# Performance work log

Hardware: AMD Instinct MI355X
Metric: run time of the kernel (lower is better)

The kernel has to match this reference:

```python
import math
import jax, jax.numpy as jnp
import numpy as np

# ---- matryoshka config (matches init_kwargs) ----
NUM_HEADS = 16
KV_GROUPS = 4
KV_REPEATS = NUM_HEADS // KV_GROUPS
QK_SIZES = [32, 64, 128]      # output_sizes // num_heads
HEAD_SIZES = [32, 64, 128]
D_MODEL = 2048
NEG_INF = -1e9


def _heads_reorder_indices(num_heads, sizes, reverse=False):
    parts = [[] for _ in range(num_heads)]
    offset, prev = 0, 0
    for size in sizes:
        seg = size - prev
        for h in range(num_heads):
            parts[h].append(np.arange(offset, offset + seg))
            offset += seg
        prev = size
    reorder = np.concatenate([a for head in parts for a in head])
    if reverse:
        rev = np.empty_like(reorder)
        rev[reorder] = np.arange(len(reorder))
        reorder = rev
    return jnp.asarray(reorder, dtype=jnp.int32)

Q_REORDER = _heads_reorder_indices(NUM_HEADS, QK_SIZES)
K_REORDER = _heads_reorder_indices(KV_GROUPS, QK_SIZES)
V_REORDER = _heads_reorder_indices(KV_GROUPS, HEAD_SIZES)
O_REORDER = _heads_reorder_indices(NUM_HEADS, HEAD_SIZES, reverse=True)


def setup_inputs() -> dict:
    key = jax.random.key(0)
    ks = jax.random.split(key, 9)
    B, S = 2, 1024
    dq = NUM_HEADS * QK_SIZES[-1]      # 2048
    dkv_q = KV_GROUPS * QK_SIZES[-1]   # 512
    dkv_v = KV_GROUPS * HEAD_SIZES[-1] # 512
    dout = NUM_HEADS * HEAD_SIZES[-1]  # 2048
    s = 0.02
    return {
        "x": jax.random.normal(ks[0], (B, S, D_MODEL), jnp.float32),
        "mask": jnp.tril(jnp.ones((S, S), jnp.bool_)),
        "Wq": jax.random.normal(ks[1], (D_MODEL, dq), jnp.float32) * s,
        "bq": jnp.zeros((dq,), jnp.float32),
        "Wk": jax.random.normal(ks[2], (D_MODEL, dkv_q), jnp.float32) * s,
        "bk": jnp.zeros((dkv_q,), jnp.float32),
        "Wv": jax.random.normal(ks[3], (D_MODEL, dkv_v), jnp.float32) * s,
        "bv": jnp.zeros((dkv_v,), jnp.float32),
        "Wo": jax.random.normal(ks[4], (dout, D_MODEL), jnp.float32) * s,
        "bo": jnp.zeros((D_MODEL,), jnp.float32),
    }


def reference(x, mask, Wq, bq, Wk, bk, Wv, bv, Wo, bo):
    B, S, _ = x.shape
    H, G, R = NUM_HEADS, KV_GROUPS, KV_REPEATS
    Dq, Dh = QK_SIZES[-1], HEAD_SIZES[-1]

    # matryoshka projections (full-size forward) + buffer-indexed reorder
    q = (x @ Wq + bq)[..., Q_REORDER]
    k = (x @ Wk + bk)[..., K_REORDER]
    v = (x @ Wv + bv)[..., V_REORDER]

    q = q.reshape(B, S, H, Dq).transpose(0, 2, 1, 3)   # [B,H,S,Dq]
    k = k.reshape(B, S, G, Dq).transpose(0, 2, 1, 3)   # [B,G,S,Dq]
    v = v.reshape(B, S, G, Dh).transpose(0, 2, 1, 3)   # [B,G,S,Dh]

    # GQA expansion: each group repeated kv_repeats times consecutively
    k = jnp.repeat(k, R, axis=1)  # [B,H,S,Dq]
    v = jnp.repeat(v, R, axis=1)  # [B,H,S,Dh]

    add_mask = jnp.where(mask, 0.0, NEG_INF).astype(x.dtype)  # [S,S]

    xs = []
    dp_cum = 0.0
    prev_qk, prev_hd = 0, 0
    for qk, hd in zip(QK_SIZES, HEAD_SIZES):
        # dot product over the NEW qk segment, accumulated over prefixes
        dp = jnp.einsum('bhqd,bhkd->bhqk', q[..., prev_qk:qk], k[..., prev_qk:qk])
        dp_cum = dp_cum + dp
        logits = dp_cum * (1.0 / math.sqrt(qk)) + add_mask
        attn = jax.nn.softmax(logits, axis=-1)
        # output only the NEW value segment for this nesting level
        xs.append(jnp.einsum('bhqk,bhkd->bhqd', attn, v[..., prev_hd:hd]))
        prev_qk, prev_hd = qk, hd

    out = jnp.concatenate(xs, axis=-1)                 # [B,H,S,Dh]
    out = out.transpose(0, 2, 1, 3).reshape(B, S, H * Dh)
    out = out[..., O_REORDER]
    return out @ Wo + bo
```

## Files before the change

kernel.cpp:

```cpp
#include <hip/hip_runtime.h>

typedef __attribute__((ext_vector_type(8))) __bf16 bf16x8;
typedef __attribute__((ext_vector_type(8))) unsigned short u16x8;
typedef __attribute__((ext_vector_type(4))) float f32x4;

#define XBOFF 0
#define WQKVOFF (XBOFF + 2048 * 2048)
#define WOOFF   (WQKVOFF + 3072 * 2048)
#define QOFF    (WOOFF + 2048 * 2048)
#define KOFF    (QOFF + 2048 * 2048)
#define VTOFF   (KOFF + 2048 * 512)
#define AOFF    (VTOFF + 2048 * 512)
__device__ __align__(16) ushort g_scratch[AOFF + 2048 * 2048];

__device__ __forceinline__ int nest_map(int n, int H) {
    int h = n >> 7, j = n & 127;
    if (j < 32) return h * 32 + j;
    if (j < 64) return H * 32 + h * 32 + (j - 32);
    return H * 64 + h * 64 + (j - 64);
}

__device__ __forceinline__ ushort f2bf(float f) {
    unsigned u = __builtin_bit_cast(unsigned, f);
    u += 0x7fffu + ((u >> 16) & 1u);
    return (ushort)(u >> 16);
}
__device__ __forceinline__ bf16x8 ld_frag(const ushort* p) {
    return __builtin_bit_cast(bf16x8, *(const u16x8*)p);
}
__device__ __forceinline__ void glds16(const ushort* g, ushort* s) {
    __builtin_amdgcn_global_load_lds(
        (const __attribute__((address_space(1))) void*)g,
        (__attribute__((address_space(3))) void*)s, 16, 0, 0);
}

__global__ __launch_bounds__(256) void prep_kernel(
    const float* __restrict__ x,
    const float* __restrict__ Wq, const float* __restrict__ Wk,
    const float* __restrict__ Wv, const float* __restrict__ Wo)
{
    const int bx = blockIdx.x;
    const int tid = threadIdx.x;

    if (bx < 2048) {
        size_t i = ((size_t)bx * 256 + tid) * 8;
        float4 f0 = *(const float4*)&x[i];
        float4 f1 = *(const float4*)&x[i + 4];
        union { uint4 v; ushort u[8]; } a;
        a.u[0] = f2bf(f0.x); a.u[1] = f2bf(f0.y); a.u[2] = f2bf(f0.z); a.u[3] = f2bf(f0.w);
        a.u[4] = f2bf(f1.x); a.u[5] = f2bf(f1.y); a.u[6] = f2bf(f1.z); a.u[7] = f2bf(f1.w);
        *(uint4*)&g_scratch[XBOFF + i] = a.v;
        return;
    }

    const float* W; int rowlen, H, mode, dstoff, t;
    if (bx < 3072)      { W = Wq; rowlen = 2048; H = 16; mode = 0; dstoff = WQKVOFF;               t = bx - 2048; }
    else if (bx < 3328) { W = Wk; rowlen = 512;  H = 4;  mode = 0; dstoff = WQKVOFF + 2048 * 2048; t = bx - 3072; }
    else if (bx < 3584) { W = Wv; rowlen = 512;  H = 4;  mode = 0; dstoff = WQKVOFF + 2560 * 2048; t = bx - 3328; }
    else                { W = Wo; rowlen = 2048; H = 16; mode = 1; dstoff = WOOFF;                 t = bx - 3584; }
    const int k0 = (t & 31) * 64;
    const int n0 = (t >> 5) * 64;

    __shared__ ushort T[64][66];
    const int r = tid >> 3, oct = tid & 7;

    #pragma unroll
    for (int rep = 0; rep < 2; ++rep) {
        int rr = r + rep * 32;
        int wrow = mode ? nest_map(k0 + rr, 16) : (k0 + rr);
        int wcol = mode ? (n0 + oct * 8) : nest_map(n0 + oct * 8, H);
        float4 f0 = *(const float4*)&W[(size_t)wrow * rowlen + wcol];
        float4 f1 = *(const float4*)&W[(size_t)wrow * rowlen + wcol + 4];
        ushort* d = &T[rr][oct * 8];
        d[0] = f2bf(f0.x); d[1] = f2bf(f0.y); d[2] = f2bf(f0.z); d[3] = f2bf(f0.w);
        d[4] = f2bf(f1.x); d[5] = f2bf(f1.y); d[6] = f2bf(f1.z); d[7] = f2bf(f1.w);
    }
    __syncthreads();
    #pragma unroll
    for (int rep = 0; rep < 2; ++rep) {
        int rr = r + rep * 32;
        union { uint4 v; ushort u[8]; } cv;
        #pragma unroll
        for (int i = 0; i < 8; ++i) cv.u[i] = T[oct * 8 + i][rr];
        *(uint4*)&g_scratch[dstoff + (size_t)(n0 + rr) * 2048 + k0 + oct * 8] = cv.v;
    }
}

__global__ __launch_bounds__(256) void gemm128_kernel(
    const float* __restrict__ b0, const float* __restrict__ b1,
    const float* __restrict__ b2, float* __restrict__ oext, int mode)
{
    __shared__ __align__(16) ushort SH[128 * 64 + 64 * 64];
    ushort* As = SH;
    ushort* Bs = SH + 128 * 64;

    const int gx = gridDim.x;
    const int nwg = gx * gridDim.y;
    const int id = blockIdx.x + gx * blockIdx.y;
    const int id2 = (id & 7) * (nwg >> 3) + (id >> 3);
    const int m_idx = id2 / gx;
    const int n_idx = id2 - m_idx * gx;
    const int n0 = n_idx * 64;
    const int m0 = m_idx * 128;

    const int tid = threadIdx.x;
    const int lane = tid & 63, wid = tid >> 6;
    const int wm = wid & 1, wn = wid >> 1;
    const int quad = lane >> 4, l16 = lane & 15;

    const ushort* A  = g_scratch + (mode ? AOFF : XBOFF);
    const ushort* Bt = g_scratch + (mode ? WOOFF : WQKVOFF);

    const bool vpath = (mode == 0) && (n0 >= 2560);
    const float* bias; ushort* outS = nullptr; int c0, oldim, H;
    if (mode == 1)      { bias = b0; c0 = n0; oldim = 2048; H = 0; }
    else if (n0 < 2048) { bias = b0; outS = g_scratch + QOFF; c0 = n0;        oldim = 2048; H = 16; }
    else if (n0 < 2560) { bias = b1; outS = g_scratch + KOFF; c0 = n0 - 2048; oldim = 512;  H = 4; }
    else                { bias = b2; outS = nullptr;          c0 = n0 - 2560; oldim = 512;  H = 4; }

    const int lrow = lane >> 3;
    const int lchunk = (lane & 7) ^ (lrow & 7);

    f32x4 acc[4][2];
    #pragma unroll
    for (int a = 0; a < 4; ++a)
        #pragma unroll
        for (int c = 0; c < 2; ++c) acc[a][c] = f32x4{0.f, 0.f, 0.f, 0.f};

    for (int kt = 0; kt < 32; ++kt) {
        const int k0 = kt * 64;
        #pragma unroll
        for (int it = 0; it < 4; ++it) {
            int rb = it * 32 + wid * 8;
            int r  = rb + lrow;
            glds16(&A[(size_t)(m0 + r) * 2048 + k0 + lchunk * 8], &As[rb * 64]);
        }
        #pragma unroll
        for (int it = 0; it < 2; ++it) {
            int rb = it * 32 + wid * 8;
            int r  = rb + lrow;
            glds16(&Bt[(size_t)(n0 + r) * 2048 + k0 + lchunk * 8], &Bs[rb * 64]);
        }
        __syncthreads();
        #pragma unroll
        for (int kc = 0; kc < 2; ++kc) {
            bf16x8 af[4], bf[2];
            #pragma unroll
            for (int s = 0; s < 4; ++s) {
                int ra = wm * 64 + s * 16 + l16;
                int ch = kc * 4 + quad;
                af[s] = ld_frag(&As[ra * 64 + ((ch ^ (ra & 7)) * 8)]);
            }
            #pragma unroll
            for (int s = 0; s < 2; ++s) {
                int rbv = wn * 32 + s * 16 + l16;
                int ch = kc * 4 + quad;
                bf[s] = ld_frag(&Bs[rbv * 64 + ((ch ^ (rbv & 7)) * 8)]);
            }
            #pragma unroll
            for (int sm = 0; sm < 4; ++sm)
                #pragma unroll
                for (int sn = 0; sn < 2; ++sn)
                    acc[sm][sn] = __builtin_amdgcn_mfma_f32_16x16x32_bf16(
                        af[sm], bf[sn], acc[sm][sn], 0, 0, 0);
        }
        __syncthreads();
    }

    if (vpath) {
        #pragma unroll
        for (int sm = 0; sm < 4; ++sm)
        #pragma unroll
        for (int sn = 0; sn < 2; ++sn)
        #pragma unroll
        for (int i = 0; i < 4; ++i) {
            int r = wm * 64 + sm * 16 + quad * 4 + i;
            int loc = wn * 32 + sn * 16 + l16;
            float v = acc[sm][sn][i] + bias[nest_map(c0 + loc, 4)];
            SH[loc * 128 + (r ^ ((loc & 7) << 3))] = f2bf(v);
        }
        __syncthreads();
        const int dloc = tid >> 2;
        const int qcol = (tid & 3) * 32;
        const int gg = c0 >> 7, din = (c0 & 127);
        const int bb = m0 >> 10, sb = m0 & 1023;
        ushort* vt = g_scratch + VTOFF;
        #pragma unroll
        for (int j = 0; j < 4; ++j) {
            int r = qcol + j * 8;
            uint4 v = *(uint4*)&SH[dloc * 128 + (r ^ ((dloc & 7) << 3))];
            *(uint4*)&vt[((size_t)((bb * 4 + gg) * 128 + din + dloc)) * 1024 + sb + r] = v;
        }
    } else {
        #pragma unroll
        for (int sm = 0; sm < 4; ++sm)
        #pragma unroll
        for (int sn = 0; sn < 2; ++sn)
        #pragma unroll
        for (int i = 0; i < 4; ++i) {
            int row = m0 + wm * 64 + sm * 16 + quad * 4 + i;
            int loc = wn * 32 + sn * 16 + l16;
            float v = acc[sm][sn][i];
            if (mode == 1) {
                oext[(size_t)row * 2048 + c0 + loc] = v + bias[c0 + loc];
            } else {
                v += bias[nest_map(c0 + loc, H)];
                outS[(size_t)row * oldim + c0 + loc] = f2bf(v);
            }
        }
    }
}

__global__ __launch_bounds__(256) void attn_kernel()
{
    const ushort* qb = g_scratch + QOFF;
    const ushort* kb = g_scratch + KOFF;
    const ushort* vt = g_scratch + VTOFF;
    ushort* att = g_scratch + AOFF;

    __shared__ __align__(16) ushort Ks[64 * 128];
    __shared__ __align__(16) ushort Vt[128 * 64];
    __shared__ __align__(16) ushort Ps[64 * 64];

    const int x = blockIdx.x, h = blockIdx.y, b = blockIdx.z;
    const int ks_half = x >> 1;
    const int qt = ((x ^ b) & 1) ? ks_half : 15 - ks_half;
    const int g = h >> 2;
    const int q0 = qt * 64;
    const int tid = threadIdx.x;
    const int lane = tid & 63, w = tid >> 6;
    const int quad = lane >> 4, l16 = lane & 15;

    bf16x8 qa[4];
    {
        const ushort* qrow =
            qb + ((size_t)((b * 1024 + q0 + w * 16 + l16) * 16 + h)) * 128;
        #pragma unroll
        for (int kc = 0; kc < 4; ++kc)
            qa[kc] = ld_frag(qrow + kc * 32 + quad * 8);
    }

    float m_s[3][4], l_s[3][4];
    #pragma unroll
    for (int l = 0; l < 3; ++l)
        #pragma unroll
        for (int i = 0; i < 4; ++i) { m_s[l][i] = -1e9f; l_s[l][i] = 0.0f; }
    f32x4 oacc[8];
    #pragma unroll
    for (int t2 = 0; t2 < 8; ++t2) oacc[t2] = f32x4{0.f, 0.f, 0.f, 0.f};
    const f32x4 fz = {0.f, 0.f, 0.f, 0.f};

    for (int kt = 0; kt <= qt; ++kt) {
        const int k0 = kt * 64;
        {
            int r16 = tid >> 4, oct16 = tid & 15;
            #pragma unroll
            for (int rep = 0; rep < 4; ++rep) {
                int row = r16 + rep * 16;
                *(uint4*)&Ks[row * 128 + ((oct16 ^ (row & 7)) * 8)] =
                    *(const uint4*)&kb[(size_t)((b * 1024 + k0 + row) * 4 + g) * 128 + oct16 * 8];
            }
            int oct = tid & 7, dr = tid >> 3;
            #pragma unroll
            for (int rep = 0; rep < 4; ++rep) {
                int d = dr + rep * 32;
                *(uint4*)&Vt[d * 64 + ((oct ^ (d & 7)) * 8)] =
                    *(const uint4*)&vt[((size_t)((b * 4 + g) * 128 + d)) * 1024 + k0 + oct * 8];
            }
        }
        __syncthreads();

        const bool diag = (kt == qt);

        f32x4 s0[4], s1[4], s2[4];
        __builtin_amdgcn_s_setprio(1);
        #pragma unroll
        for (int n = 0; n < 4; ++n) {
            int r = n * 16 + l16;
            s0[n] = __builtin_amdgcn_mfma_f32_16x16x32_bf16(
                qa[0], ld_frag(&Ks[r * 128 + (((0 + quad) ^ (r & 7)) * 8)]), fz, 0, 0, 0);
        }
        #pragma unroll
        for (int n = 0; n < 4; ++n) {
            int r = n * 16 + l16;
            s1[n] = __builtin_amdgcn_mfma_f32_16x16x32_bf16(
                qa[1], ld_frag(&Ks[r * 128 + (((4 + quad) ^ (r & 7)) * 8)]), s0[n], 0, 0, 0);
        }
        #pragma unroll
        for (int n = 0; n < 4; ++n) {
            int r = n * 16 + l16;
            s2[n] = __builtin_amdgcn_mfma_f32_16x16x32_bf16(
                qa[2], ld_frag(&Ks[r * 128 + (((8 + quad) ^ (r & 7)) * 8)]), s1[n], 0, 0, 0);
        }
        #pragma unroll
        for (int n = 0; n < 4; ++n) {
            int r = n * 16 + l16;
            s2[n] = __builtin_amdgcn_mfma_f32_16x16x32_bf16(
                qa[3], ld_frag(&Ks[r * 128 + (((12 + quad) ^ (r & 7)) * 8)]), s2[n], 0, 0, 0);
        }
        __builtin_amdgcn_s_setprio(0);

        float sv[3][4][4], mx[3][4];
        #pragma unroll
        for (int l = 0; l < 3; ++l)
            #pragma unroll
            for (int i = 0; i < 4; ++i) mx[l][i] = -1e9f;
        #pragma unroll
        for (int n = 0; n < 4; ++n)
            #pragma unroll
            for (int i = 0; i < 4; ++i) {
                bool msk = diag &&
                    (k0 + n * 16 + l16 > q0 + w * 16 + quad * 4 + i);
                float x0 = msk ? -1e9f : s0[n][i] * 0.1767766953f;
                float x1 = msk ? -1e9f : s1[n][i] * 0.125f;
                float x2 = msk ? -1e9f : s2[n][i] * 0.0883883476f;
                sv[0][n][i] = x0; mx[0][i] = fmaxf(mx[0][i], x0);
                sv[1][n][i] = x1; mx[1][i] = fmaxf(mx[1][i], x1);
                sv[2][n][i] = x2; mx[2][i] = fmaxf(mx[2][i], x2);
            }
        #pragma unroll
        for (int d = 1; d < 16; d <<= 1)
            #pragma unroll
            for (int l = 0; l < 3; ++l)
                #pragma unroll
                for (int i = 0; i < 4; ++i)
                    mx[l][i] = fmaxf(mx[l][i], __shfl_xor(mx[l][i], d, 64));
        float al[3][4], rs[3][4];
        #pragma unroll
        for (int l = 0; l < 3; ++l)
            #pragma unroll
            for (int i = 0; i < 4; ++i) {
                float mn = fmaxf(m_s[l][i], mx[l][i]);
                al[l][i] = __expf(m_s[l][i] - mn);
                m_s[l][i] = mn;
                rs[l][i] = 0.f;
            }
        #pragma unroll
        for (int n = 0; n < 4; ++n)
            #pragma unroll
            for (int l = 0; l < 3; ++l)
                #pragma unroll
                for (int i = 0; i < 4; ++i) {
                    float p = __expf(sv[l][n][i] - m_s[l][i]);
                    sv[l][n][i] = p;
                    rs[l][i] += p;
                }
        #pragma unroll
        for (int d = 1; d < 16; d <<= 1)
            #pragma unroll
            for (int l = 0; l < 3; ++l)
                #pragma unroll
                for (int i = 0; i < 4; ++i)
                    rs[l][i] += __shfl_xor(rs[l][i], d, 64);
        #pragma unroll
        for (int l = 0; l < 3; ++l)
            #pragma unroll
            for (int i = 0; i < 4; ++i)
                l_s[l][i] = l_s[l][i] * al[l][i] + rs[l][i];
        #pragma unroll
        for (int t = 0; t < 8; ++t) {
            int lvl = (t < 2) ? 0 : (t < 4) ? 1 : 2;
            #pragma unroll
            for (int i = 0; i < 4; ++i) oacc[t][i] *= al[lvl][i];
        }

        const int obase[3] = {0, 2, 4}, onts[3] = {2, 2, 4}, voffs[3] = {0, 32, 64};
        #pragma unroll
        for (int l = 0; l < 3; ++l) {
            #pragma unroll
            for (int n = 0; n < 4; ++n)
                #pragma unroll
                for (int i = 0; i < 4; ++i) {
                    int prow = w * 16 + quad * 4 + i;
                    int col = n * 16 + l16;
                    Ps[prow * 64 + ((((col >> 3) ^ (prow & 7)) << 3) | (col & 7))] =
                        f2bf(sv[l][n][i]);
                }
            __builtin_amdgcn_s_setprio(1);
            #pragma unroll
            for (int kc = 0; kc < 2; ++kc) {
                int prow = w * 16 + l16;
                bf16x8 pa = ld_frag(&Ps[prow * 64 + (((kc * 4 + quad) ^ (prow & 7)) * 8)]);
                #pragma unroll
                for (int t = 0; t < 4; ++t) {
                    if (t < onts[l]) {
                        int vd = voffs[l] + t * 16 + l16;
                        bf16x8 vf = ld_frag(&Vt[vd * 64 + (((kc * 4 + quad) ^ (vd & 7)) * 8)]);
                        oacc[obase[l] + t] = __builtin_amdgcn_mfma_f32_16x16x32_bf16(
                            pa, vf, oacc[obase[l] + t], 0, 0, 0);
                    }
                }
            }
            __builtin_amdgcn_s_setprio(0);
        }
        __syncthreads();
    }

    float inv[3][4];
    #pragma unroll
    for (int l = 0; l < 3; ++l)
        #pragma unroll
        for (int i = 0; i < 4; ++i) {
            float L = l_s[l][i];
            inv[l][i] = (L > 0.f) ? (1.0f / L) : 0.f;
        }
    #pragma unroll
    for (int t = 0; t < 8; ++t) {
        int lvl = (t < 2) ? 0 : (t < 4) ? 1 : 2;
        #pragma unroll
        for (int i = 0; i < 4; ++i) {
            int srow = q0 + w * 16 + quad * 4 + i;
            att[(size_t)((b * 1024 + srow) * 16 + h) * 128 + t * 16 + l16] =
                f2bf(oacc[t][i] * inv[lvl][i]);
        }
    }
}

extern "C" void kernel_launch(void* const* d_in, const int* in_sizes, int n_in,
                              void* d_out, int out_size, void* d_ws, size_t ws_size,
                              hipStream_t stream)
{
    const float* x  = (const float*)d_in[0];
    const float* Wq = (const float*)d_in[2];
    const float* bq = (const float*)d_in[3];
    const float* Wk = (const float*)d_in[4];
    const float* bk = (const float*)d_in[5];
    const float* Wv = (const float*)d_in[6];
    const float* bv = (const float*)d_in[7];
    const float* Wo = (const float*)d_in[8];
    const float* bo = (const float*)d_in[9];
    float* out = (float*)d_out;
    (void)d_ws; (void)ws_size;

    dim3 blk(256, 1, 1);
    hipLaunchKernelGGL(prep_kernel, dim3(4608), blk, 0, stream, x, Wq, Wk, Wv, Wo);
    hipLaunchKernelGGL(gemm128_kernel, dim3(48, 16), blk, 0, stream,
                       bq, bk, bv, (float*)nullptr, 0);
    hipLaunchKernelGGL(attn_kernel, dim3(16, 16, 2), blk, 0, stream);
    hipLaunchKernelGGL(gemm128_kernel, dim3(32, 16), blk, 0, stream,
                       bo, nullptr, nullptr, out, 1);
}
```

Before: 277.9 us.

## Split attention blocks into 32-row halves and compute row sums via MFMA

```diff
diff --git a/kernel.cpp b/kernel.cpp
--- a/kernel.cpp
+++ b/kernel.cpp
@@ -211,7 +211,7 @@
     }
 }
 
-__global__ __launch_bounds__(256) void attn_kernel()
+__global__ __launch_bounds__(128) void attn_kernel()
 {
     const ushort* qb = g_scratch + QOFF;
     const ushort* kb = g_scratch + KOFF;
@@ -220,13 +220,14 @@
 
     __shared__ __align__(16) ushort Ks[64 * 128];
     __shared__ __align__(16) ushort Vt[128 * 64];
-    __shared__ __align__(16) ushort Ps[64 * 64];
-
-    const int x = blockIdx.x, h = blockIdx.y, b = blockIdx.z;
-    const int ks_half = x >> 1;
-    const int qt = ((x ^ b) & 1) ? ks_half : 15 - ks_half;
+    __shared__ __align__(16) ushort Ps[32 * 64];
+
+    const int x = blockIdx.x, y = blockIdx.y, b = blockIdx.z;
+    const int h = x >> 1, half = x & 1;
+    const int qt = (y < 8) ? (15 - y) : (y - 8);
     const int g = h >> 2;
     const int q0 = qt * 64;
+    const int r0 = q0 + half * 32;
     const int tid = threadIdx.x;
     const int lane = tid & 63, w = tid >> 6;
     const int quad = lane >> 4, l16 = lane & 15;
@@ -234,7 +235,7 @@
     bf16x8 qa[4];
     {
         const ushort* qrow =
-            qb + ((size_t)((b * 1024 + q0 + w * 16 + l16) * 16 + h)) * 128;
+            qb + ((size_t)((b * 1024 + r0 + w * 16 + l16) * 16 + h)) * 128;
         #pragma unroll
         for (int kc = 0; kc < 4; ++kc)
             qa[kc] = ld_frag(qrow + kc * 32 + quad * 8);
@@ -249,21 +250,23 @@
     #pragma unroll
     for (int t2 = 0; t2 < 8; ++t2) oacc[t2] = f32x4{0.f, 0.f, 0.f, 0.f};
     const f32x4 fz = {0.f, 0.f, 0.f, 0.f};
+    const bf16x8 ones = __builtin_bit_cast(bf16x8, u16x8{
+        0x3F80, 0x3F80, 0x3F80, 0x3F80, 0x3F80, 0x3F80, 0x3F80, 0x3F80});
 
     for (int kt = 0; kt <= qt; ++kt) {
         const int k0 = kt * 64;
         {
             int r16 = tid >> 4, oct16 = tid & 15;
             #pragma unroll
-            for (int rep = 0; rep < 4; ++rep) {
-                int row = r16 + rep * 16;
+            for (int rep = 0; rep < 8; ++rep) {
+                int row = r16 + rep * 8;
                 *(uint4*)&Ks[row * 128 + ((oct16 ^ (row & 7)) * 8)] =
                     *(const uint4*)&kb[(size_t)((b * 1024 + k0 + row) * 4 + g) * 128 + oct16 * 8];
             }
             int oct = tid & 7, dr = tid >> 3;
             #pragma unroll
-            for (int rep = 0; rep < 4; ++rep) {
-                int d = dr + rep * 32;
+            for (int rep = 0; rep < 8; ++rep) {
+                int d = dr + rep * 16;
                 *(uint4*)&Vt[d * 64 + ((oct ^ (d & 7)) * 8)] =
                     *(const uint4*)&vt[((size_t)((b * 4 + g) * 128 + d)) * 1024 + k0 + oct * 8];
             }
@@ -310,7 +313,7 @@
             #pragma unroll
             for (int i = 0; i < 4; ++i) {
                 bool msk = diag &&
-                    (k0 + n * 16 + l16 > q0 + w * 16 + quad * 4 + i);
+                    (k0 + n * 16 + l16 > r0 + w * 16 + quad * 4 + i);
                 float x0 = msk ? -1e9f : s0[n][i] * 0.1767766953f;
                 float x1 = msk ? -1e9f : s1[n][i] * 0.125f;
                 float x2 = msk ? -1e9f : s2[n][i] * 0.0883883476f;
@@ -325,7 +328,7 @@
                 #pragma unroll
                 for (int i = 0; i < 4; ++i)
                     mx[l][i] = fmaxf(mx[l][i], __shfl_xor(mx[l][i], d, 64));
-        float al[3][4], rs[3][4];
+        float al[3][4];
         #pragma unroll
         for (int l = 0; l < 3; ++l)
             #pragma unroll
@@ -333,30 +336,14 @@
                 float mn = fmaxf(m_s[l][i], mx[l][i]);
                 al[l][i] = __expf(m_s[l][i] - mn);
                 m_s[l][i] = mn;
-                rs[l][i] = 0.f;
             }
         #pragma unroll
         for (int n = 0; n < 4; ++n)
-            #pragma unroll
-            for (int l = 0; l < 3; ++l)
-                #pragma unroll
-                for (int i = 0; i < 4; ++i) {
-                    float p = __expf(sv[l][n][i] - m_s[l][i]);
-                    sv[l][n][i] = p;
-                    rs[l][i] += p;
-                }
-        #pragma unroll
-        for (int d = 1; d < 16; d <<= 1)
             #pragma unroll
             for (int l = 0; l < 3; ++l)
                 #pragma unroll
                 for (int i = 0; i < 4; ++i)
-                    rs[l][i] += __shfl_xor(rs[l][i], d, 64);
-        #pragma unroll
-        for (int l = 0; l < 3; ++l)
-            #pragma unroll
-            for (int i = 0; i < 4; ++i)
-                l_s[l][i] = l_s[l][i] * al[l][i] + rs[l][i];
+                    sv[l][n][i] = __expf(sv[l][n][i] - m_s[l][i]);
         #pragma unroll
         for (int t = 0; t < 8; ++t) {
             int lvl = (t < 2) ? 0 : (t < 4) ? 1 : 2;
@@ -364,6 +351,7 @@
             for (int i = 0; i < 4; ++i) oacc[t][i] *= al[lvl][i];
         }
 
+        f32x4 racc[3];
         const int obase[3] = {0, 2, 4}, onts[3] = {2, 2, 4}, voffs[3] = {0, 32, 64};
         #pragma unroll
         for (int l = 0; l < 3; ++l) {
@@ -376,11 +364,14 @@
                     Ps[prow * 64 + ((((col >> 3) ^ (prow & 7)) << 3) | (col & 7))] =
                         f2bf(sv[l][n][i]);
                 }
+            racc[l] = fz;
             __builtin_amdgcn_s_setprio(1);
             #pragma unroll
             for (int kc = 0; kc < 2; ++kc) {
                 int prow = w * 16 + l16;
                 bf16x8 pa = ld_frag(&Ps[prow * 64 + (((kc * 4 + quad) ^ (prow & 7)) * 8)]);
+                racc[l] = __builtin_amdgcn_mfma_f32_16x16x32_bf16(
+                    pa, ones, racc[l], 0, 0, 0);
                 #pragma unroll
                 for (int t = 0; t < 4; ++t) {
                     if (t < onts[l]) {
@@ -393,6 +384,11 @@
             }
             __builtin_amdgcn_s_setprio(0);
         }
+        #pragma unroll
+        for (int l = 0; l < 3; ++l)
+            #pragma unroll
+            for (int i = 0; i < 4; ++i)
+                l_s[l][i] = l_s[l][i] * al[l][i] + racc[l][i];
         __syncthreads();
     }
 
@@ -409,7 +405,7 @@
         int lvl = (t < 2) ? 0 : (t < 4) ? 1 : 2;
         #pragma unroll
         for (int i = 0; i < 4; ++i) {
-            int srow = q0 + w * 16 + quad * 4 + i;
+            int srow = r0 + w * 16 + quad * 4 + i;
             att[(size_t)((b * 1024 + srow) * 16 + h) * 128 + t * 16 + l16] =
                 f2bf(oacc[t][i] * inv[lvl][i]);
         }
@@ -432,11 +428,10 @@
     float* out = (float*)d_out;
     (void)d_ws; (void)ws_size;
 
-    dim3 blk(256, 1, 1);
-    hipLaunchKernelGGL(prep_kernel, dim3(4608), blk, 0, stream, x, Wq, Wk, Wv, Wo);
-    hipLaunchKernelGGL(gemm128_kernel, dim3(48, 16), blk, 0, stream,
+    hipLaunchKernelGGL(prep_kernel, dim3(4608), dim3(256), 0, stream, x, Wq, Wk, Wv, Wo);
+    hipLaunchKernelGGL(gemm128_kernel, dim3(48, 16), dim3(256), 0, stream,
                        bq, bk, bv, (float*)nullptr, 0);
-    hipLaunchKernelGGL(attn_kernel, dim3(16, 16, 2), blk, 0, stream);
-    hipLaunchKernelGGL(gemm128_kernel, dim3(32, 16), blk, 0, stream,
+    hipLaunchKernelGGL(attn_kernel, dim3(32, 16, 2), dim3(128), 0, stream);
+    hipLaunchKernelGGL(gemm128_kernel, dim3(32, 16), dim3(256), 0, stream,
                        bo, nullptr, nullptr, out, 1);
 }
```

Result: slower. 288.5 us (+3.8%).

## Double-buffer GEMM LDS tiles and compute softmax row sums via MFMA

Applied to the files above, without the earlier changes.

```diff
diff --git a/kernel.cpp b/kernel.cpp
--- a/kernel.cpp
+++ b/kernel.cpp
@@ -90,9 +90,7 @@
     const float* __restrict__ b0, const float* __restrict__ b1,
     const float* __restrict__ b2, float* __restrict__ oext, int mode)
 {
-    __shared__ __align__(16) ushort SH[128 * 64 + 64 * 64];
-    ushort* As = SH;
-    ushort* Bs = SH + 128 * 64;
+    __shared__ __align__(16) ushort SH[2 * 12288];
 
     const int gx = gridDim.x;
     const int nwg = gx * gridDim.y;
@@ -127,21 +125,33 @@
         #pragma unroll
         for (int c = 0; c < 2; ++c) acc[a][c] = f32x4{0.f, 0.f, 0.f, 0.f};
 
-    for (int kt = 0; kt < 32; ++kt) {
+    auto STAGE = [&](int buf, int kt) {
         const int k0 = kt * 64;
+        ushort* as_ = SH + buf * 12288;
+        ushort* bs_ = as_ + 8192;
         #pragma unroll
         for (int it = 0; it < 4; ++it) {
             int rb = it * 32 + wid * 8;
             int r  = rb + lrow;
-            glds16(&A[(size_t)(m0 + r) * 2048 + k0 + lchunk * 8], &As[rb * 64]);
+            glds16(&A[(size_t)(m0 + r) * 2048 + k0 + lchunk * 8], &as_[rb * 64]);
         }
         #pragma unroll
         for (int it = 0; it < 2; ++it) {
             int rb = it * 32 + wid * 8;
             int r  = rb + lrow;
-            glds16(&Bt[(size_t)(n0 + r) * 2048 + k0 + lchunk * 8], &Bs[rb * 64]);
-        }
-        __syncthreads();
+            glds16(&Bt[(size_t)(n0 + r) * 2048 + k0 + lchunk * 8], &bs_[rb * 64]);
+        }
+    };
+
+    STAGE(0, 0);
+    __syncthreads();
+
+    for (int kt = 0; kt < 32; ++kt) {
+        const int cur = kt & 1;
+        if (kt < 31) STAGE(cur ^ 1, kt + 1);
+
+        const ushort* as_ = SH + cur * 12288;
+        const ushort* bs_ = as_ + 8192;
         #pragma unroll
         for (int kc = 0; kc < 2; ++kc) {
             bf16x8 af[4], bf[2];
@@ -149,13 +159,13 @@
             for (int s = 0; s < 4; ++s) {
                 int ra = wm * 64 + s * 16 + l16;
                 int ch = kc * 4 + quad;
-                af[s] = ld_frag(&As[ra * 64 + ((ch ^ (ra & 7)) * 8)]);
+                af[s] = ld_frag(&as_[ra * 64 + ((ch ^ (ra & 7)) * 8)]);
             }
             #pragma unroll
             for (int s = 0; s < 2; ++s) {
                 int rbv = wn * 32 + s * 16 + l16;
                 int ch = kc * 4 + quad;
-                bf[s] = ld_frag(&Bs[rbv * 64 + ((ch ^ (rbv & 7)) * 8)]);
+                bf[s] = ld_frag(&bs_[rbv * 64 + ((ch ^ (rbv & 7)) * 8)]);
             }
             #pragma unroll
             for (int sm = 0; sm < 4; ++sm)
@@ -249,6 +259,8 @@
     #pragma unroll
     for (int t2 = 0; t2 < 8; ++t2) oacc[t2] = f32x4{0.f, 0.f, 0.f, 0.f};
     const f32x4 fz = {0.f, 0.f, 0.f, 0.f};
+    const bf16x8 ones = __builtin_bit_cast(bf16x8, u16x8{
+        0x3F80, 0x3F80, 0x3F80, 0x3F80, 0x3F80, 0x3F80, 0x3F80, 0x3F80});
 
     for (int kt = 0; kt <= qt; ++kt) {
         const int k0 = kt * 64;
@@ -325,7 +337,7 @@
                 #pragma unroll
                 for (int i = 0; i < 4; ++i)
                     mx[l][i] = fmaxf(mx[l][i], __shfl_xor(mx[l][i], d, 64));
-        float al[3][4], rs[3][4];
+        float al[3][4];
         #pragma unroll
         for (int l = 0; l < 3; ++l)
             #pragma unroll
@@ -333,30 +345,14 @@
                 float mn = fmaxf(m_s[l][i], mx[l][i]);
                 al[l][i] = __expf(m_s[l][i] - mn);
                 m_s[l][i] = mn;
-                rs[l][i] = 0.f;
             }
         #pragma unroll
         for (int n = 0; n < 4; ++n)
-            #pragma unroll
-            for (int l = 0; l < 3; ++l)
-                #pragma unroll
-                for (int i = 0; i < 4; ++i) {
-                    float p = __expf(sv[l][n][i] - m_s[l][i]);
-                    sv[l][n][i] = p;
-                    rs[l][i] += p;
-                }
-        #pragma unroll
-        for (int d = 1; d < 16; d <<= 1)
             #pragma unroll
             for (int l = 0; l < 3; ++l)
                 #pragma unroll
                 for (int i = 0; i < 4; ++i)
-                    rs[l][i] += __shfl_xor(rs[l][i], d, 64);
-        #pragma unroll
-        for (int l = 0; l < 3; ++l)
-            #pragma unroll
-            for (int i = 0; i < 4; ++i)
-                l_s[l][i] = l_s[l][i] * al[l][i] + rs[l][i];
+                    sv[l][n][i] = __expf(sv[l][n][i] - m_s[l][i]);
         #pragma unroll
         for (int t = 0; t < 8; ++t) {
             int lvl = (t < 2) ? 0 : (t < 4) ? 1 : 2;
@@ -364,6 +360,7 @@
             for (int i = 0; i < 4; ++i) oacc[t][i] *= al[lvl][i];
         }
 
+        f32x4 racc[3];
         const int obase[3] = {0, 2, 4}, onts[3] = {2, 2, 4}, voffs[3] = {0, 32, 64};
         #pragma unroll
         for (int l = 0; l < 3; ++l) {
@@ -376,11 +373,14 @@
                     Ps[prow * 64 + ((((col >> 3) ^ (prow & 7)) << 3) | (col & 7))] =
                         f2bf(sv[l][n][i]);
                 }
+            racc[l] = fz;
             __builtin_amdgcn_s_setprio(1);
             #pragma unroll
             for (int kc = 0; kc < 2; ++kc) {
                 int prow = w * 16 + l16;
                 bf16x8 pa = ld_frag(&Ps[prow * 64 + (((kc * 4 + quad) ^ (prow & 7)) * 8)]);
+                racc[l] = __builtin_amdgcn_mfma_f32_16x16x32_bf16(
+                    pa, ones, racc[l], 0, 0, 0);
                 #pragma unroll
                 for (int t = 0; t < 4; ++t) {
                     if (t < onts[l]) {
@@ -393,6 +393,11 @@
             }
             __builtin_amdgcn_s_setprio(0);
         }
+        #pragma unroll
+        for (int l = 0; l < 3; ++l)
+            #pragma unroll
+            for (int i = 0; i < 4; ++i)
+                l_s[l][i] = l_s[l][i] * al[l][i] + racc[l][i];
         __syncthreads();
     }
 
```

After: 265.7 us. 1.05x faster.
